# Kernel optimization log

Measured on AMD Instinct MI355X. Metric: run time of the kernel, lower is better.

Reference implementation:

```python
import jax, jax.numpy as jnp
import numpy as np

B = 1024
S_OUT, S_IN, D_IN = 30, 17, 3
H = 4
DKQ_I, DV_I, HID_I, OUT_I = 6, 8, 256, 64
DKQ_O, DV_O, HID_O = 64, 64, 1024
OUT_O = 36 * S_OUT  # 1080


def _mha(x, wq, bq, wk, bk, wv, bv, dkq):
    """Vectorized multi-head self-attention over all heads at once.
    x: [..., P, d_in]; wq/wk: [H, d_in, dkq]; wv: [H, d_in, dv].
    Returns context [..., H, P, dv] (matches torch stack+permute ordering)."""
    q = jnp.einsum('...pd,hdk->...hpk', x, wq) + bq[:, None, :]
    k = jnp.einsum('...pd,hdk->...hpk', x, wk) + bk[:, None, :]
    v = jnp.einsum('...pd,hdv->...hpv', x, wv) + bv[:, None, :]
    scores = jnp.einsum('...hpk,...hqk->...hpq', q, k) / jnp.sqrt(jnp.asarray(dkq, x.dtype))
    attn = jax.nn.softmax(scores, axis=-1)
    return jnp.einsum('...hpq,...hqv->...hpv', attn, v)


def _ml(ctx, w1, b1, w2, b2):
    """MultiHeadLinearLayer: per-head fc1+tanh (shared weights), concat heads, fc2.
    ctx: [..., H, P, dv] -> [..., out]."""
    lead = ctx.shape[:-3]
    flat = ctx.reshape(*lead, H, -1)            # [..., H, P*dv]
    h = jnp.tanh(flat @ w1 + b1)                # [..., H, hidden]
    h = h.reshape(*lead, -1)                    # [..., H*hidden]
    return h @ w2 + b2


def setup_inputs() -> dict:
    key = jax.random.key(0)
    ks = iter(jax.random.split(key, 32))
    n = lambda shape, s=0.05: jax.random.normal(next(ks), shape, dtype=jnp.float32) * s
    inp = {
        'x': jax.random.normal(next(ks), (B, S_OUT, S_IN, D_IN), dtype=jnp.float32),
        # inner multi-head attention (4 heads, stacked weights)
        'iwq': n((H, D_IN, DKQ_I)), 'ibq': n((H, DKQ_I)),
        'iwk': n((H, D_IN, DKQ_I)), 'ibk': n((H, DKQ_I)),
        'iwv': n((H, D_IN, DV_I)),  'ibv': n((H, DV_I)),
        # inner MultiHeadLinearLayer
        'iw1': n((S_IN * DV_I, HID_I)), 'ib1': n((HID_I,)),
        'iw2': n((H * HID_I, OUT_I)),   'ib2': n((OUT_I,)),
        # outer multi-head attention
        'owq': n((H, OUT_I, DKQ_O)), 'obq': n((H, DKQ_O)),
        'owk': n((H, OUT_I, DKQ_O)), 'obk': n((H, DKQ_O)),
        'owv': n((H, OUT_I, DV_O)),  'obv': n((H, DV_O)),
        # outer MultiHeadLinearLayer
        'ow1': n((S_OUT * DV_O, HID_O)), 'ob1': n((HID_O,)),
        'ow2': n((H * HID_O, OUT_O)),    'ob2': n((OUT_O,)),
    }
    return inp


def reference(x, iwq, ibq, iwk, ibk, iwv, ibv, iw1, ib1, iw2, ib2,
              owq, obq, owk, obk, owv, obv, ow1, ob1, ow2, ob2):
    b = x.shape[0]
    # Inner attention applied to all 30 outer positions at once (replaces python loop)
    ctx_i = _mha(x, iwq, ibq, iwk, ibk, iwv, ibv, DKQ_I)      # [B,30,H,17,8]
    seq = _ml(ctx_i, iw1, ib1, iw2, ib2)                       # [B,30,64]
    # Outer attention over the 30-step sequence
    ctx_o = _mha(seq, owq, obq, owk, obk, owv, obv, DKQ_O)     # [B,H,30,64]
    out = _ml(ctx_o, ow1, ob1, ow2, ob2)                       # [B,1080]
    return out.reshape(b, S_OUT, 12, 3)
```

## Files before the change

### kernel.cpp

```cpp
#include <hip/hip_runtime.h>


typedef _Float16 f16x8 __attribute__((ext_vector_type(8)));
typedef _Float16 f16x4 __attribute__((ext_vector_type(4)));
typedef float    f32x4 __attribute__((ext_vector_type(4)));
typedef float    f32x16 __attribute__((ext_vector_type(16)));

union F16x8u { f16x8 v; f16x4 q[2]; };

__device__ inline float tanh_fast(float x) {
    float ax = fabsf(x);
    float e  = __expf(2.0f * ax);
    float r  = 1.0f - 2.0f / (e + 1.0f);
    return copysignf(r, x);
}

__device__ inline f32x16 zero16() {
    f32x16 z;
    #pragma unroll
    for (int i = 0; i < 16; i++) z[i] = 0.f;
    return z;
}

__global__ __launch_bounds__(256) void k_prep_frags(
    const float* __restrict__ iwq, const float* __restrict__ ibq,
    const float* __restrict__ iwk, const float* __restrict__ ibk,
    const float* __restrict__ iwv, const float* __restrict__ ibv,
    _Float16* __restrict__ wqf, _Float16* __restrict__ wkf, _Float16* __restrict__ wvf)
{
    const float SC = 0.40824829046386307f;
    for (int i = threadIdx.x; i < 512; i += 256) {
        const int lanev = i >> 3, jj = i & 7;
        const int n = lanev & 31, grp = lanev >> 5;
        const int h = n >> 3, dk = n & 7;
        float q = 0.f, k = 0.f, v = 0.f;
        if (!grp) {
            if (jj < 3) {
                if (dk < 6) { q = iwq[h*18 + jj*6 + dk] * SC; k = iwk[h*18 + jj*6 + dk]; }
                v = iwv[h*24 + jj*8 + dk];
            } else if (jj == 3) {
                if (dk < 6) { q = ibq[h*6 + dk] * SC; k = ibk[h*6 + dk]; }
                v = ibv[h*8 + dk];
            }
        }
        wqf[i] = (_Float16)q; wkf[i] = (_Float16)k; wvf[i] = (_Float16)v;
    }
}

__global__ __launch_bounds__(256) void k_tcastT(
    const float* __restrict__ W, _Float16* __restrict__ Wt,
    int K, int N, int Kpad)
{
    __shared__ _Float16 tile[64][65];
    const int k0 = blockIdx.x * 64, n0 = blockIdx.y * 64;
    for (int i = threadIdx.x; i < 4096; i += 256) {
        const int r = i >> 6, c = i & 63;
        const int k = k0 + r, n = n0 + c;
        float v = (k < K && n < N) ? W[(size_t)k * N + n] : 0.f;
        tile[c][r] = (_Float16)v;
    }
    __syncthreads();
    for (int i = threadIdx.x; i < 4096; i += 256) {
        const int r = i >> 6, c = i & 63;
        Wt[(size_t)(n0 + r) * Kpad + k0 + c] = tile[r][c];
    }
}

__global__ void k_tcast_iw1(const float* __restrict__ iw1, _Float16* __restrict__ iw1t)
{
    const int n = blockIdx.x;
    const int t = threadIdx.x;
    const int dv = t / 20, p = t % 20;
    float v = (p < 17) ? iw1[(p*8 + dv) * 256 + n] : 0.f;
    iw1t[n * 160 + t] = (_Float16)v;
}

__global__ __launch_bounds__(256) void k_tcast_h(
    const float* __restrict__ W, _Float16* __restrict__ Wt)
{
    const int h = blockIdx.y;
    const int idx = blockIdx.x * 256 + threadIdx.x;
    const int n = idx >> 6, k = idx & 63;
    Wt[h * 4096 + n * 64 + k] = (_Float16)W[h * 4096 + k * 64 + n];
}

__global__ __launch_bounds__(256, 3) void k_inner_attn_mfma(
    const float* __restrict__ x,
    const _Float16* __restrict__ wqf, const _Float16* __restrict__ wkf,
    const _Float16* __restrict__ wvf,
    _Float16* __restrict__ flat)
{
    __shared__ __align__(16) _Float16 lds[4][5248];
    const int t = threadIdx.x, lane = t & 63, w = t >> 6;
    const int l31 = lane & 31, grp = lane >> 5;
    const int bs = blockIdx.x * 4 + w;
    _Float16* kq  = &lds[w][0];
    _Float16* qq  = &lds[w][1152];
    _Float16* vt  = &lds[w][2304];
    _Float16* pf  = &lds[w][3456];
    _Float16* fo2 = &lds[w][4608];

    f16x8 xf;
    #pragma unroll
    for (int i = 0; i < 8; i++) xf[i] = (_Float16)0.f;
    if (grp == 0 && l31 < 17) {
        const float* xr = x + (size_t)bs * 51 + l31 * 3;
        xf[0] = (_Float16)xr[0];
        xf[1] = (_Float16)xr[1];
        xf[2] = (_Float16)xr[2];
        xf[3] = (_Float16)1.0f;
    }
    const f16x8 wq8 = *(const f16x8*)&wqf[lane * 8];
    const f16x8 wk8 = *(const f16x8*)&wkf[lane * 8];
    const f16x8 wv8 = *(const f16x8*)&wvf[lane * 8];

    f32x16 kt = __builtin_amdgcn_mfma_f32_32x32x16_f16(wk8, xf, zero16(), 0, 0, 0);
    f32x16 qt = __builtin_amdgcn_mfma_f32_32x32x16_f16(wq8, xf, zero16(), 0, 0, 0);
    f32x16 vv = __builtin_amdgcn_mfma_f32_32x32x16_f16(xf, wv8, zero16(), 0, 0, 0);

    #pragma unroll
    for (int qd = 0; qd < 4; qd++) {
        const int base = 8 * qd + 4 * grp;
        f16x4 a, b, c;
        #pragma unroll
        for (int i = 0; i < 4; i++) {
            a[i] = (_Float16)kt[4*qd + i];
            b[i] = (_Float16)qt[4*qd + i];
            c[i] = (_Float16)vv[4*qd + i];
        }
        *(f16x4*)&kq[l31 * 36 + base] = a;
        *(f16x4*)&qq[l31 * 36 + base] = b;
        *(f16x4*)&vt[l31 * 36 + base] = c;
    }

    #pragma unroll
    for (int h = 0; h < 4; h++) {
        F16x8u ka, qb;
        #pragma unroll
        for (int i = 0; i < 8; i++) { ka.v[i] = (_Float16)0.f; qb.v[i] = (_Float16)0.f; }
        if (grp == 0) {
            ka.q[0] = *(const f16x4*)&kq[l31 * 36 + h * 8];
            ka.q[1] = *(const f16x4*)&kq[l31 * 36 + h * 8 + 4];
            qb.q[0] = *(const f16x4*)&qq[l31 * 36 + h * 8];
            qb.q[1] = *(const f16x4*)&qq[l31 * 36 + h * 8 + 4];
        }
        f32x16 s = __builtin_amdgcn_mfma_f32_32x32x16_f16(ka.v, qb.v, zero16(), 0, 0, 0);

        float mx = -1e30f;
        #pragma unroll
        for (int r = 0; r < 16; r++) {
            const bool val = (r < 8) || (r == 8 && grp == 0);
            if (val) mx = fmaxf(mx, s[r]);
        }
        mx = fmaxf(mx, __shfl_xor(mx, 32));
        float e[16], sum = 0.f;
        #pragma unroll
        for (int r = 0; r < 16; r++) {
            const bool val = (r < 8) || (r == 8 && grp == 0);
            e[r] = val ? __expf(s[r] - mx) : 0.f;
            sum += e[r];
        }
        sum += __shfl_xor(sum, 32);
        const float inv = __builtin_amdgcn_rcpf(sum);
        #pragma unroll
        for (int qd = 0; qd < 4; qd++) {
            f16x4 pk;
            #pragma unroll
            for (int i = 0; i < 4; i++) pk[i] = (_Float16)(e[4*qd + i] * inv);
            *(f16x4*)&pf[l31 * 36 + 8 * qd + 4 * grp] = pk;
        }

        F16x8u pa1, pa2, vb1, vb2;
        pa1.q[0] = *(const f16x4*)&pf[l31 * 36 + grp * 8];
        pa1.q[1] = *(const f16x4*)&pf[l31 * 36 + grp * 8 + 4];
        pa2.q[0] = *(const f16x4*)&pf[l31 * 36 + 16 + grp * 8];
        pa2.q[1] = *(const f16x4*)&pf[l31 * 36 + 16 + grp * 8 + 4];
        const int vr = (h * 8 + (l31 & 7)) * 36;
        vb1.q[0] = *(const f16x4*)&vt[vr + grp * 8];
        vb1.q[1] = *(const f16x4*)&vt[vr + grp * 8 + 4];
        vb2.q[0] = *(const f16x4*)&vt[vr + 16 + grp * 8];
        vb2.q[1] = *(const f16x4*)&vt[vr + 16 + grp * 8 + 4];
        f32x16 c = __builtin_amdgcn_mfma_f32_32x32x16_f16(pa1.v, vb1.v, zero16(), 0, 0, 0);
        c = __builtin_amdgcn_mfma_f32_32x32x16_f16(pa2.v, vb2.v, c, 0, 0, 0);

        if (l31 < 8) {
            #pragma unroll
            for (int qd = 0; qd < 4; qd++) {
                const int jb = 8 * qd + 4 * grp;
                if (jb < 20) {
                    f16x4 ck;
                    #pragma unroll
                    for (int i = 0; i < 4; i++) ck[i] = (_Float16)c[4*qd + i];
                    *(f16x4*)&fo2[h * 160 + l31 * 20 + jb] = ck;
                }
            }
        }
    }

    _Float16* fg = flat + (size_t)bs * 640;
    *(f16x8*)&fg[lane * 8] = *(const f16x8*)&fo2[lane * 8];
    if (lane < 16)
        *(f16x8*)&fg[512 + lane * 8] = *(const f16x8*)&fo2[512 + lane * 8];
}

__global__ __launch_bounds__(256) void k_inner_ml_mfma(
    const _Float16* __restrict__ flat,
    const _Float16* __restrict__ iw1t,
    const _Float16* __restrict__ iw2t,
    const float* __restrict__ ib1, const float* __restrict__ ib2,
    float* __restrict__ seq)
{
    __shared__ __align__(16) _Float16 h1l[32][1032];
    float* red = (float*)&h1l[0][0];
    const int t = threadIdx.x, lane = t & 63, w = t >> 6;
    const int q = lane >> 4, ml = lane & 15;
    const int m0  = blockIdx.x * 128;
    const int bs0 = blockIdx.x * 32;

    for (int p = 0; p < 2; p++) {
        f32x4 acc[4][4];
        #pragma unroll
        for (int mi = 0; mi < 4; mi++)
            #pragma unroll
            for (int ni = 0; ni < 4; ni++) acc[mi][ni] = (f32x4){0.f,0.f,0.f,0.f};
        for (int ks = 0; ks < 5; ks++) {
            const int k = ks * 32 + q * 8;
            f16x8 a[4], b[4];
            #pragma unroll
            for (int mi = 0; mi < 4; mi++)
                a[mi] = *(const f16x8*)&flat[(size_t)(m0 + p*64 + mi*16 + ml) * 160 + k];
            #pragma unroll
            for (int ni = 0; ni < 4; ni++)
                b[ni] = *(const f16x8*)&iw1t[(size_t)(w*64 + ni*16 + ml) * 160 + k];
            #pragma unroll
            for (int mi = 0; mi < 4; mi++)
                #pragma unroll
                for (int ni = 0; ni < 4; ni++)
                    acc[mi][ni] = __builtin_amdgcn_mfma_f32_16x16x32_f16(a[mi], b[ni], acc[mi][ni], 0, 0, 0);
        }
        #pragma unroll
        for (int mi = 0; mi < 4; mi++)
            #pragma unroll
            for (int ni = 0; ni < 4; ni++)
                #pragma unroll
                for (int r = 0; r < 4; r++) {
                    const int row = p*64 + mi*16 + q*4 + r;
                    const int col = w*64 + ni*16 + ml;
                    const int bs_l = row >> 2, h = row & 3;
                    h1l[bs_l][h*256 + col] = (_Float16)tanh_fast(acc[mi][ni][r] + ib1[col]);
                }
    }
    __syncthreads();

    f32x4 a2[2][4];
    #pragma unroll
    for (int mi = 0; mi < 2; mi++)
        #pragma unroll
        for (int ni = 0; ni < 4; ni++) a2[mi][ni] = (f32x4){0.f,0.f,0.f,0.f};
    for (int ks = 0; ks < 8; ks++) {
        const int k = w * 256 + ks * 32 + q * 8;
        f16x8 a[2], b[4];
        #pragma unroll
        for (int mi = 0; mi < 2; mi++)
            a[mi] = *(const f16x8*)&h1l[mi*16 + ml][k];
        #pragma unroll
        for (int ni = 0; ni < 4; ni++)
            b[ni] = *(const f16x8*)&iw2t[(size_t)(ni*16 + ml) * 1024 + k];
        #pragma unroll
        for (int mi = 0; mi < 2; mi++)
            #pragma unroll
            for (int ni = 0; ni < 4; ni++)
                a2[mi][ni] = __builtin_amdgcn_mfma_f32_16x16x32_f16(a[mi], b[ni], a2[mi][ni], 0, 0, 0);
    }
    __syncthreads();
    #pragma unroll
    for (int mi = 0; mi < 2; mi++)
        #pragma unroll
        for (int ni = 0; ni < 4; ni++)
            #pragma unroll
            for (int r = 0; r < 4; r++) {
                const int row = mi*16 + q*4 + r;
                const int col = ni*16 + ml;
                red[(size_t)w*2048 + row*64 + col] = a2[mi][ni][r];
            }
    __syncthreads();
    for (int i = t; i < 2048; i += 256) {
        const int row = i >> 6, col = i & 63;
        float s = red[i] + red[2048 + i] + red[4096 + i] + red[6144 + i] + ib2[col];
        seq[(size_t)(bs0 + row) * 64 + col] = s;
    }
}

__device__ inline void oa_proj_rows(
    const _Float16 (*seqf)[72], const _Float16* __restrict__ wt,
    const float* __restrict__ bias, _Float16 (*dst)[72], int q, int ml)
{
    f32x4 acc[2][4];
    #pragma unroll
    for (int mi = 0; mi < 2; mi++)
        #pragma unroll
        for (int ni = 0; ni < 4; ni++) acc[mi][ni] = (f32x4){0.f,0.f,0.f,0.f};
    #pragma unroll
    for (int k0 = 0; k0 < 64; k0 += 32) {
        f16x8 a[2], bb[4];
        #pragma unroll
        for (int mi = 0; mi < 2; mi++) a[mi] = *(const f16x8*)&seqf[mi*16 + ml][k0 + q*8];
        #pragma unroll
        for (int ni = 0; ni < 4; ni++) bb[ni] = *(const f16x8*)&wt[(size_t)(ni*16 + ml)*64 + k0 + q*8];
        #pragma unroll
        for (int mi = 0; mi < 2; mi++)
            #pragma unroll
            for (int ni = 0; ni < 4; ni++)
                acc[mi][ni] = __builtin_amdgcn_mfma_f32_16x16x32_f16(a[mi], bb[ni], acc[mi][ni], 0, 0, 0);
    }
    #pragma unroll
    for (int ni = 0; ni < 4; ni++) {
        const float bi = bias[ni*16 + ml];
        #pragma unroll
        for (int mi = 0; mi < 2; mi++)
            #pragma unroll
            for (int r = 0; r < 4; r++)
                dst[mi*16 + q*4 + r][ni*16 + ml] = (_Float16)(acc[mi][ni][r] + bi);
    }
}

__device__ inline void oa_proj_t(
    const _Float16 (*seqf)[72], const _Float16* __restrict__ wt,
    const float* __restrict__ bias, _Float16 (*dstT)[40], int q, int ml)
{
    f32x4 acc[2][4];
    #pragma unroll
    for (int mi = 0; mi < 2; mi++)
        #pragma unroll
        for (int ni = 0; ni < 4; ni++) acc[mi][ni] = (f32x4){0.f,0.f,0.f,0.f};
    #pragma unroll
    for (int k0 = 0; k0 < 64; k0 += 32) {
        f16x8 a[2], bb[4];
        #pragma unroll
        for (int mi = 0; mi < 2; mi++) a[mi] = *(const f16x8*)&seqf[mi*16 + ml][k0 + q*8];
        #pragma unroll
        for (int ni = 0; ni < 4; ni++) bb[ni] = *(const f16x8*)&wt[(size_t)(ni*16 + ml)*64 + k0 + q*8];
        #pragma unroll
        for (int mi = 0; mi < 2; mi++)
            #pragma unroll
            for (int ni = 0; ni < 4; ni++)
                acc[mi][ni] = __builtin_amdgcn_mfma_f32_16x16x32_f16(a[mi], bb[ni], acc[mi][ni], 0, 0, 0);
    }
    #pragma unroll
    for (int ni = 0; ni < 4; ni++) {
        const float bi = bias[ni*16 + ml];
        #pragma unroll
        for (int mi = 0; mi < 2; mi++)
            #pragma unroll
            for (int r = 0; r < 4; r++)
                dstT[ni*16 + ml][mi*16 + q*4 + r] = (_Float16)(acc[mi][ni][r] + bi);
    }
}

__global__ __launch_bounds__(256) void k_outer_attn_mfma(
    const float* __restrict__ seq,
    const _Float16* __restrict__ owqt,
    const _Float16* __restrict__ owkt,
    const _Float16* __restrict__ owvt,
    const float* __restrict__ obq, const float* __restrict__ obk,
    const float* __restrict__ obv,
    _Float16* __restrict__ ctxo)
{
    __shared__ __align__(16) _Float16 seqf[32][72];
    __shared__ __align__(16) _Float16 qf[4][32][72];
    __shared__ __align__(16) _Float16 kf[4][32][72];
    __shared__ __align__(16) _Float16 vt[4][64][40];
    __shared__ __align__(16) _Float16 pf[4][32][40];
    const int t = threadIdx.x, lane = t & 63, w = t >> 6;
    const int q = lane >> 4, ml = lane & 15;
    const int b = blockIdx.x;

    const float* sb = seq + (size_t)b * 1920;
    for (int i = t; i < 2048; i += 256) {
        const int row = i >> 6, col = i & 63;
        seqf[row][col] = (_Float16)(row < 30 ? sb[row*64 + col] : 0.0f);
    }
    __syncthreads();

    oa_proj_rows(seqf, owqt + w*4096, obq + w*64, qf[w], q, ml);
    oa_proj_rows(seqf, owkt + w*4096, obk + w*64, kf[w], q, ml);
    oa_proj_t   (seqf, owvt + w*4096, obv + w*64, vt[w], q, ml);
    __syncthreads();

    f32x4 sc[2][2];
    #pragma unroll
    for (int mi = 0; mi < 2; mi++)
        #pragma unroll
        for (int ni = 0; ni < 2; ni++) sc[mi][ni] = (f32x4){0.f,0.f,0.f,0.f};
    #pragma unroll
    for (int k0 = 0; k0 < 64; k0 += 32) {
        f16x8 aq[2], bk[2];
        #pragma unroll
        for (int mi = 0; mi < 2; mi++) aq[mi] = *(const f16x8*)&qf[w][mi*16 + ml][k0 + q*8];
        #pragma unroll
        for (int ni = 0; ni < 2; ni++) bk[ni] = *(const f16x8*)&kf[w][ni*16 + ml][k0 + q*8];
        #pragma unroll
        for (int mi = 0; mi < 2; mi++)
            #pragma unroll
            for (int ni = 0; ni < 2; ni++)
                sc[mi][ni] = __builtin_amdgcn_mfma_f32_16x16x32_f16(aq[mi], bk[ni], sc[mi][ni], 0, 0, 0);
    }

    const bool maskhi = (ml >= 14);
    #pragma unroll
    for (int mi = 0; mi < 2; mi++) {
        #pragma unroll
        for (int r = 0; r < 4; r++) {
            const float s0 = sc[mi][0][r] * 0.125f;
            const float s1 = maskhi ? -1e30f : sc[mi][1][r] * 0.125f;
            float mx = fmaxf(s0, s1);
            #pragma unroll
            for (int off = 1; off < 16; off <<= 1) mx = fmaxf(mx, __shfl_xor(mx, off, 64));
            const float e0 = __expf(s0 - mx);
            const float e1 = __expf(s1 - mx);
            float sm = e0 + e1;
            #pragma unroll
            for (int off = 1; off < 16; off <<= 1) sm += __shfl_xor(sm, off, 64);
            const float inv = 1.0f / sm;
            pf[w][mi*16 + q*4 + r][ml]      = (_Float16)(e0 * inv);
            pf[w][mi*16 + q*4 + r][16 + ml] = (_Float16)(e1 * inv);
        }
    }
    __syncthreads();

    f16x8 ap[2], bv[4];
    #pragma unroll
    for (int mi = 0; mi < 2; mi++) ap[mi] = *(const f16x8*)&pf[w][mi*16 + ml][q*8];
    #pragma unroll
    for (int ni = 0; ni < 4; ni++) bv[ni] = *(const f16x8*)&vt[w][ni*16 + ml][q*8];
    f32x4 oa[2][4];
    #pragma unroll
    for (int mi = 0; mi < 2; mi++)
        #pragma unroll
        for (int ni = 0; ni < 4; ni++) {
            oa[mi][ni] = (f32x4){0.f,0.f,0.f,0.f};
            oa[mi][ni] = __builtin_amdgcn_mfma_f32_16x16x32_f16(ap[mi], bv[ni], oa[mi][ni], 0, 0, 0);
        }

    _Float16* co = ctxo + (size_t)(b*4 + w) * 1920;
    #pragma unroll
    for (int mi = 0; mi < 2; mi++)
        #pragma unroll
        for (int r = 0; r < 4; r++) {
            const int row = mi*16 + q*4 + r;
            if (row < 30) {
                #pragma unroll
                for (int ni = 0; ni < 4; ni++)
                    co[row*64 + ni*16 + ml] = (_Float16)oa[mi][ni][r];
            }
        }
}

__global__ __launch_bounds__(128) void k_outer_fc1_mfma(
    const _Float16* __restrict__ ctxo,
    const _Float16* __restrict__ ow1t,
    const float* __restrict__ ob1,
    _Float16* __restrict__ hout)
{
    __shared__ float red[2][64][65];
    const int t = threadIdx.x, lane = t & 63, w = t >> 6;
    const int q = lane >> 4, ml = lane & 15;
    const int M0 = (blockIdx.x >> 4) * 64;
    const int N0 = (blockIdx.x & 15) * 64;
    f32x4 acc[4][4];
    #pragma unroll
    for (int mi = 0; mi < 4; mi++)
        #pragma unroll
        for (int ni = 0; ni < 4; ni++) acc[mi][ni] = (f32x4){0.f,0.f,0.f,0.f};
    for (int ks = 0; ks < 30; ks++) {
        const int k = w * 960 + ks * 32 + q * 8;
        f16x8 a[4], b[4];
        #pragma unroll
        for (int mi = 0; mi < 4; mi++)
            a[mi] = *(const f16x8*)&ctxo[(size_t)(M0 + mi*16 + ml) * 1920 + k];
        #pragma unroll
        for (int ni = 0; ni < 4; ni++)
            b[ni] = *(const f16x8*)&ow1t[(size_t)(N0 + ni*16 + ml) * 1920 + k];
        #pragma unroll
        for (int mi = 0; mi < 4; mi++)
            #pragma unroll
            for (int ni = 0; ni < 4; ni++)
                acc[mi][ni] = __builtin_amdgcn_mfma_f32_16x16x32_f16(a[mi], b[ni], acc[mi][ni], 0, 0, 0);
    }
    #pragma unroll
    for (int mi = 0; mi < 4; mi++)
        #pragma unroll
        for (int ni = 0; ni < 4; ni++)
            #pragma unroll
            for (int r = 0; r < 4; r++)
                red[w][mi*16 + q*4 + r][ni*16 + ml] = acc[mi][ni][r];
    __syncthreads();
    for (int i = t; i < 4096; i += 128) {
        const int row = i >> 6, col = i & 63;
        const float s = red[0][row][col] + red[1][row][col] + ob1[N0 + col];
        hout[(size_t)(M0 + row) * 1024 + N0 + col] = (_Float16)tanh_fast(s);
    }
}

__global__ __launch_bounds__(256) void k_outer_fc2_mfma(
    const _Float16* __restrict__ hout,
    const _Float16* __restrict__ ow2t,
    const float* __restrict__ ob2,
    float* __restrict__ out)
{
    __shared__ float red[4][32][65];
    const int t = threadIdx.x, lane = t & 63, w = t >> 6;
    const int q = lane >> 4, ml = lane & 15;
    const int M0 = (blockIdx.x / 17) * 32;
    const int N0 = (blockIdx.x % 17) * 64;
    f32x4 acc[2][4];
    #pragma unroll
    for (int mi = 0; mi < 2; mi++)
        #pragma unroll
        for (int ni = 0; ni < 4; ni++) acc[mi][ni] = (f32x4){0.f,0.f,0.f,0.f};
    for (int ks = 0; ks < 32; ks++) {
        const int k = w * 1024 + ks * 32 + q * 8;
        f16x8 a[2], b[4];
        #pragma unroll
        for (int mi = 0; mi < 2; mi++)
            a[mi] = *(const f16x8*)&hout[(size_t)(M0 + mi*16 + ml) * 4096 + k];
        #pragma unroll
        for (int ni = 0; ni < 4; ni++)
            b[ni] = *(const f16x8*)&ow2t[(size_t)(N0 + ni*16 + ml) * 4096 + k];
        #pragma unroll
        for (int mi = 0; mi < 2; mi++)
            #pragma unroll
            for (int ni = 0; ni < 4; ni++)
                acc[mi][ni] = __builtin_amdgcn_mfma_f32_16x16x32_f16(a[mi], b[ni], acc[mi][ni], 0, 0, 0);
    }
    #pragma unroll
    for (int mi = 0; mi < 2; mi++)
        #pragma unroll
        for (int ni = 0; ni < 4; ni++)
            #pragma unroll
            for (int r = 0; r < 4; r++)
                red[w][mi*16 + q*4 + r][ni*16 + ml] = acc[mi][ni][r];
    __syncthreads();
    for (int i = t; i < 2048; i += 256) {
        const int row = i >> 6, col = i & 63;
        const int n = N0 + col;
        if (n < 1080) {
            float s = red[0][row][col] + red[1][row][col] + red[2][row][col] + red[3][row][col] + ob2[n];
            out[(size_t)(M0 + row) * 1080 + n] = s;
        }
    }
}

extern "C" void kernel_launch(void* const* d_in, const int* in_sizes, int n_in,
                              void* d_out, int out_size, void* d_ws, size_t ws_size,
                              hipStream_t stream) {
    const float* x   = (const float*)d_in[0];
    const float* iwq = (const float*)d_in[1];
    const float* ibq = (const float*)d_in[2];
    const float* iwk = (const float*)d_in[3];
    const float* ibk = (const float*)d_in[4];
    const float* iwv = (const float*)d_in[5];
    const float* ibv = (const float*)d_in[6];
    const float* iw1 = (const float*)d_in[7];
    const float* ib1 = (const float*)d_in[8];
    const float* iw2 = (const float*)d_in[9];
    const float* ib2 = (const float*)d_in[10];
    const float* owq = (const float*)d_in[11];
    const float* obq = (const float*)d_in[12];
    const float* owk = (const float*)d_in[13];
    const float* obk = (const float*)d_in[14];
    const float* owv = (const float*)d_in[15];
    const float* obv = (const float*)d_in[16];
    const float* ow1 = (const float*)d_in[17];
    const float* ob1 = (const float*)d_in[18];
    const float* ow2 = (const float*)d_in[19];
    const float* ob2 = (const float*)d_in[20];

    char* ws = (char*)d_ws;
    _Float16* iw1t   = (_Float16*)(ws + 0);
    _Float16* wqf    = (_Float16*)(ws + 98304);
    _Float16* wkf    = (_Float16*)(ws + 99328);
    _Float16* wvf    = (_Float16*)(ws + 100352);
    _Float16* iw2t   = (_Float16*)(ws + 163840);
    _Float16* ow1t   = (_Float16*)(ws + 294912);
    _Float16* ow2t   = (_Float16*)(ws + 4227072);
    _Float16* flat   = (_Float16*)(ws + 13139968);
    float*    seq    = (float*)   (ws + 52461568);
    _Float16* owqt   = (_Float16*)(ws + 60325888);
    _Float16* owkt   = (_Float16*)(ws + 60358656);
    _Float16* owvt   = (_Float16*)(ws + 60391424);
    _Float16* ctxo   = (_Float16*)(ws + 13139968);
    _Float16* houtb  = (_Float16*)(ws + 28868608);
    float*    out    = (float*)d_out;

    k_prep_frags<<<dim3(1), dim3(256), 0, stream>>>(iwq, ibq, iwk, ibk, iwv, ibv, wqf, wkf, wvf);
    k_tcast_iw1 <<<dim3(256), dim3(160), 0, stream>>>(iw1, iw1t);
    k_tcastT<<<dim3(16, 1),  dim3(256), 0, stream>>>(iw2, iw2t, 1024, 64, 1024);
    k_tcastT<<<dim3(30, 16), dim3(256), 0, stream>>>(ow1, ow1t, 1920, 1024, 1920);
    k_tcastT<<<dim3(64, 17), dim3(256), 0, stream>>>(ow2, ow2t, 4096, 1080, 4096);
    k_tcast_h<<<dim3(16, 4), dim3(256), 0, stream>>>(owq, owqt);
    k_tcast_h<<<dim3(16, 4), dim3(256), 0, stream>>>(owk, owkt);
    k_tcast_h<<<dim3(16, 4), dim3(256), 0, stream>>>(owv, owvt);

    k_inner_attn_mfma<<<dim3(7680), dim3(256), 0, stream>>>(x, wqf, wkf, wvf, flat);
    k_inner_ml_mfma  <<<dim3(960),  dim3(256), 0, stream>>>(flat, iw1t, iw2t, ib1, ib2, seq);
    k_outer_attn_mfma<<<dim3(1024), dim3(256), 0, stream>>>(seq, owqt, owkt, owvt, obq, obk, obv, ctxo);
    k_outer_fc1_mfma <<<dim3(1024), dim3(128), 0, stream>>>(ctxo, ow1t, ob1, houtb);
    k_outer_fc2_mfma <<<dim3(544),  dim3(256), 0, stream>>>(houtb, ow2t, ob2, out);
}
```

Baseline: 374.7 us.

## Fuse weight prep kernels, double-buffer GEMM loads, split-K outer fc2

Merges the eight weight-cast/transpose launches into a single block-dispatched kernel. The outer fc1 and fc2 GEMMs now prefetch the next K-step's fragments into registers while issuing MFMAs on the current step. The fc2 GEMM is split four ways along K to launch four times as many blocks. Fp32 partials go to workspace and a separate reduction kernel adds them with the bias. This targets launch overhead and low occupancy/latency exposure in fc2, at the cost of extra partial-sum memory traffic, another launch, and more registers for double-buffering.

```diff
diff --git a/kernel.cpp b/kernel.cpp
--- a/kernel.cpp
+++ b/kernel.cpp
@@ -22,66 +22,85 @@
     return z;
 }
 
-__global__ __launch_bounds__(256) void k_prep_frags(
-    const float* __restrict__ iwq, const float* __restrict__ ibq,
-    const float* __restrict__ iwk, const float* __restrict__ ibk,
-    const float* __restrict__ iwv, const float* __restrict__ ibv,
-    _Float16* __restrict__ wqf, _Float16* __restrict__ wkf, _Float16* __restrict__ wvf)
-{
-    const float SC = 0.40824829046386307f;
-    for (int i = threadIdx.x; i < 512; i += 256) {
-        const int lanev = i >> 3, jj = i & 7;
-        const int n = lanev & 31, grp = lanev >> 5;
-        const int h = n >> 3, dk = n & 7;
-        float q = 0.f, k = 0.f, v = 0.f;
-        if (!grp) {
-            if (jj < 3) {
-                if (dk < 6) { q = iwq[h*18 + jj*6 + dk] * SC; k = iwk[h*18 + jj*6 + dk]; }
-                v = iwv[h*24 + jj*8 + dk];
-            } else if (jj == 3) {
-                if (dk < 6) { q = ibq[h*6 + dk] * SC; k = ibk[h*6 + dk]; }
-                v = ibv[h*8 + dk];
-            }
-        }
-        wqf[i] = (_Float16)q; wkf[i] = (_Float16)k; wvf[i] = (_Float16)v;
-    }
-}
-
-__global__ __launch_bounds__(256) void k_tcastT(
+__device__ inline void tcast_tile(
     const float* __restrict__ W, _Float16* __restrict__ Wt,
-    int K, int N, int Kpad)
-{
-    __shared__ _Float16 tile[64][65];
-    const int k0 = blockIdx.x * 64, n0 = blockIdx.y * 64;
-    for (int i = threadIdx.x; i < 4096; i += 256) {
+    int tileIdx, int nkx, int K, int N, int Kpad,
+    _Float16 (*tile)[65], int t)
+{
+    const int kx = tileIdx % nkx, ny = tileIdx / nkx;
+    const int k0 = kx * 64, n0 = ny * 64;
+    for (int i = t; i < 4096; i += 256) {
         const int r = i >> 6, c = i & 63;
         const int k = k0 + r, n = n0 + c;
         float v = (k < K && n < N) ? W[(size_t)k * N + n] : 0.f;
         tile[c][r] = (_Float16)v;
     }
     __syncthreads();
-    for (int i = threadIdx.x; i < 4096; i += 256) {
+    for (int i = t; i < 4096; i += 256) {
         const int r = i >> 6, c = i & 63;
         Wt[(size_t)(n0 + r) * Kpad + k0 + c] = tile[r][c];
     }
 }
 
-__global__ void k_tcast_iw1(const float* __restrict__ iw1, _Float16* __restrict__ iw1t)
-{
-    const int n = blockIdx.x;
-    const int t = threadIdx.x;
-    const int dv = t / 20, p = t % 20;
-    float v = (p < 17) ? iw1[(p*8 + dv) * 256 + n] : 0.f;
-    iw1t[n * 160 + t] = (_Float16)v;
-}
-
-__global__ __launch_bounds__(256) void k_tcast_h(
-    const float* __restrict__ W, _Float16* __restrict__ Wt)
-{
-    const int h = blockIdx.y;
-    const int idx = blockIdx.x * 256 + threadIdx.x;
-    const int n = idx >> 6, k = idx & 63;
-    Wt[h * 4096 + n * 64 + k] = (_Float16)W[h * 4096 + k * 64 + n];
+__global__ __launch_bounds__(256) void k_prep_all(
+    const float* __restrict__ iwq, const float* __restrict__ ibq,
+    const float* __restrict__ iwk, const float* __restrict__ ibk,
+    const float* __restrict__ iwv, const float* __restrict__ ibv,
+    const float* __restrict__ iw1, const float* __restrict__ iw2,
+    const float* __restrict__ ow1, const float* __restrict__ ow2,
+    const float* __restrict__ owq, const float* __restrict__ owk,
+    const float* __restrict__ owv,
+    _Float16* __restrict__ wqf, _Float16* __restrict__ wkf,
+    _Float16* __restrict__ wvf,
+    _Float16* __restrict__ iw1t, _Float16* __restrict__ iw2t,
+    _Float16* __restrict__ ow1t, _Float16* __restrict__ ow2t,
+    _Float16* __restrict__ owqt, _Float16* __restrict__ owkt,
+    _Float16* __restrict__ owvt)
+{
+    __shared__ _Float16 tile[64][65];
+    const int b = blockIdx.x, t = threadIdx.x;
+    if (b == 0) {
+        const float SC = 0.40824829046386307f;
+        for (int i = t; i < 512; i += 256) {
+            const int lanev = i >> 3, jj = i & 7;
+            const int n = lanev & 31, grp = lanev >> 5;
+            const int h = n >> 3, dk = n & 7;
+            float q = 0.f, k = 0.f, v = 0.f;
+            if (!grp) {
+                if (jj < 3) {
+                    if (dk < 6) { q = iwq[h*18 + jj*6 + dk] * SC; k = iwk[h*18 + jj*6 + dk]; }
+                    v = iwv[h*24 + jj*8 + dk];
+                } else if (jj == 3) {
+                    if (dk < 6) { q = ibq[h*6 + dk] * SC; k = ibk[h*6 + dk]; }
+                    v = ibv[h*8 + dk];
+                }
+            }
+            wqf[i] = (_Float16)q; wkf[i] = (_Float16)k; wvf[i] = (_Float16)v;
+        }
+    } else if (b < 161) {
+        const int idx = (b - 1) * 256 + t;
+        if (idx < 40960) {
+            const int n = idx / 160, kp = idx - n * 160;
+            const int dv = kp / 20, p = kp - dv * 20;
+            float v = (p < 17) ? iw1[(p*8 + dv) * 256 + n] : 0.f;
+            iw1t[n * 160 + kp] = (_Float16)v;
+        }
+    } else if (b < 177) {
+        tcast_tile(iw2, iw2t, b - 161, 16, 1024, 64, 1024, tile, t);
+    } else if (b < 657) {
+        tcast_tile(ow1, ow1t, b - 177, 30, 1920, 1024, 1920, tile, t);
+    } else if (b < 1745) {
+        tcast_tile(ow2, ow2t, b - 657, 64, 4096, 1080, 4096, tile, t);
+    } else {
+        const int s = b - 1745;
+        const int mat = s >> 6, rem = s & 63;
+        const int h = rem >> 4, blk = rem & 15;
+        const int idx = blk * 256 + t;
+        const int n = idx >> 6, k = idx & 63;
+        const float* W = (mat == 0) ? owq : (mat == 1) ? owk : owv;
+        _Float16* Wt   = (mat == 0) ? owqt : (mat == 1) ? owkt : owvt;
+        Wt[h * 4096 + n * 64 + k] = (_Float16)W[h * 4096 + k * 64 + n];
+    }
 }
 
 __global__ __launch_bounds__(256, 3) void k_inner_attn_mfma(
@@ -467,25 +486,36 @@
     const int q = lane >> 4, ml = lane & 15;
     const int M0 = (blockIdx.x >> 4) * 64;
     const int N0 = (blockIdx.x & 15) * 64;
+    const int kk0 = w * 960 + q * 8;
     f32x4 acc[4][4];
     #pragma unroll
     for (int mi = 0; mi < 4; mi++)
         #pragma unroll
         for (int ni = 0; ni < 4; ni++) acc[mi][ni] = (f32x4){0.f,0.f,0.f,0.f};
+    f16x8 a[2][4], b[2][4];
+    #pragma unroll
+    for (int mi = 0; mi < 4; mi++)
+        a[0][mi] = *(const f16x8*)&ctxo[(size_t)(M0 + mi*16 + ml) * 1920 + kk0];
+    #pragma unroll
+    for (int ni = 0; ni < 4; ni++)
+        b[0][ni] = *(const f16x8*)&ow1t[(size_t)(N0 + ni*16 + ml) * 1920 + kk0];
+    #pragma unroll
     for (int ks = 0; ks < 30; ks++) {
-        const int k = w * 960 + ks * 32 + q * 8;
-        f16x8 a[4], b[4];
+        const int cur = ks & 1, nxt = cur ^ 1;
+        if (ks < 29) {
+            const int kn = kk0 + (ks + 1) * 32;
+            #pragma unroll
+            for (int mi = 0; mi < 4; mi++)
+                a[nxt][mi] = *(const f16x8*)&ctxo[(size_t)(M0 + mi*16 + ml) * 1920 + kn];
+            #pragma unroll
+            for (int ni = 0; ni < 4; ni++)
+                b[nxt][ni] = *(const f16x8*)&ow1t[(size_t)(N0 + ni*16 + ml) * 1920 + kn];
+        }
         #pragma unroll
         for (int mi = 0; mi < 4; mi++)
-            a[mi] = *(const f16x8*)&ctxo[(size_t)(M0 + mi*16 + ml) * 1920 + k];
-        #pragma unroll
-        for (int ni = 0; ni < 4; ni++)
-            b[ni] = *(const f16x8*)&ow1t[(size_t)(N0 + ni*16 + ml) * 1920 + k];
-        #pragma unroll
-        for (int mi = 0; mi < 4; mi++)
-            #pragma unroll
-            for (int ni = 0; ni < 4; ni++)
-                acc[mi][ni] = __builtin_amdgcn_mfma_f32_16x16x32_f16(a[mi], b[ni], acc[mi][ni], 0, 0, 0);
+            #pragma unroll
+            for (int ni = 0; ni < 4; ni++)
+                acc[mi][ni] = __builtin_amdgcn_mfma_f32_16x16x32_f16(a[cur][mi], b[cur][ni], acc[mi][ni], 0, 0, 0);
     }
     #pragma unroll
     for (int mi = 0; mi < 4; mi++)
@@ -505,33 +535,46 @@
 __global__ __launch_bounds__(256) void k_outer_fc2_mfma(
     const _Float16* __restrict__ hout,
     const _Float16* __restrict__ ow2t,
-    const float* __restrict__ ob2,
-    float* __restrict__ out)
+    float* __restrict__ part)
 {
     __shared__ float red[4][32][65];
     const int t = threadIdx.x, lane = t & 63, w = t >> 6;
     const int q = lane >> 4, ml = lane & 15;
-    const int M0 = (blockIdx.x / 17) * 32;
-    const int N0 = (blockIdx.x % 17) * 64;
+    const int bid = blockIdx.x;
+    const int kc = bid & 3;
+    const int rest = bid >> 2;
+    const int M0 = (rest / 17) * 32;
+    const int N0 = (rest % 17) * 64;
+    const int kk0 = kc * 1024 + w * 256 + q * 8;
     f32x4 acc[2][4];
     #pragma unroll
     for (int mi = 0; mi < 2; mi++)
         #pragma unroll
         for (int ni = 0; ni < 4; ni++) acc[mi][ni] = (f32x4){0.f,0.f,0.f,0.f};
-    for (int ks = 0; ks < 32; ks++) {
-        const int k = w * 1024 + ks * 32 + q * 8;
-        f16x8 a[2], b[4];
-        #pragma unroll
-        for (int mi = 0; mi < 2; mi++)
-            a[mi] = *(const f16x8*)&hout[(size_t)(M0 + mi*16 + ml) * 4096 + k];
-        #pragma unroll
-        for (int ni = 0; ni < 4; ni++)
-            b[ni] = *(const f16x8*)&ow2t[(size_t)(N0 + ni*16 + ml) * 4096 + k];
-        #pragma unroll
-        for (int mi = 0; mi < 2; mi++)
-            #pragma unroll
-            for (int ni = 0; ni < 4; ni++)
-                acc[mi][ni] = __builtin_amdgcn_mfma_f32_16x16x32_f16(a[mi], b[ni], acc[mi][ni], 0, 0, 0);
+    f16x8 a[2][2], b[2][4];
+    #pragma unroll
+    for (int mi = 0; mi < 2; mi++)
+        a[0][mi] = *(const f16x8*)&hout[(size_t)(M0 + mi*16 + ml) * 4096 + kk0];
+    #pragma unroll
+    for (int ni = 0; ni < 4; ni++)
+        b[0][ni] = *(const f16x8*)&ow2t[(size_t)(N0 + ni*16 + ml) * 4096 + kk0];
+    #pragma unroll
+    for (int ks = 0; ks < 8; ks++) {
+        const int cur = ks & 1, nxt = cur ^ 1;
+        if (ks < 7) {
+            const int kn = kk0 + (ks + 1) * 32;
+            #pragma unroll
+            for (int mi = 0; mi < 2; mi++)
+                a[nxt][mi] = *(const f16x8*)&hout[(size_t)(M0 + mi*16 + ml) * 4096 + kn];
+            #pragma unroll
+            for (int ni = 0; ni < 4; ni++)
+                b[nxt][ni] = *(const f16x8*)&ow2t[(size_t)(N0 + ni*16 + ml) * 4096 + kn];
+        }
+        #pragma unroll
+        for (int mi = 0; mi < 2; mi++)
+            #pragma unroll
+            for (int ni = 0; ni < 4; ni++)
+                acc[mi][ni] = __builtin_amdgcn_mfma_f32_16x16x32_f16(a[cur][mi], b[cur][ni], acc[mi][ni], 0, 0, 0);
     }
     #pragma unroll
     for (int mi = 0; mi < 2; mi++)
@@ -545,10 +588,21 @@
         const int row = i >> 6, col = i & 63;
         const int n = N0 + col;
         if (n < 1080) {
-            float s = red[0][row][col] + red[1][row][col] + red[2][row][col] + red[3][row][col] + ob2[n];
-            out[(size_t)(M0 + row) * 1080 + n] = s;
-        }
-    }
+            const float s = red[0][row][col] + red[1][row][col] + red[2][row][col] + red[3][row][col];
+            part[(size_t)kc * 1105920 + (size_t)(M0 + row) * 1080 + n] = s;
+        }
+    }
+}
+
+__global__ __launch_bounds__(256) void k_fc2_reduce(
+    const float* __restrict__ part, const float* __restrict__ ob2,
+    float* __restrict__ out)
+{
+    const int idx = blockIdx.x * 256 + threadIdx.x;
+    if (idx >= 1105920) return;
+    const int n = idx % 1080;
+    out[idx] = part[idx] + part[1105920 + idx] + part[2211840 + idx]
+             + part[3317760 + idx] + ob2[n];
 }
 
 extern "C" void kernel_launch(void* const* d_in, const int* in_sizes, int n_in,
@@ -590,21 +644,17 @@
     _Float16* owkt   = (_Float16*)(ws + 60358656);
     _Float16* owvt   = (_Float16*)(ws + 60391424);
     _Float16* ctxo   = (_Float16*)(ws + 13139968);
-    _Float16* houtb  = (_Float16*)(ws + 28868608);
+    float*    part   = (float*)   (ws + 13139968);
+    _Float16* houtb  = (_Float16*)(ws + 40000000);
     float*    out    = (float*)d_out;
 
-    k_prep_frags<<<dim3(1), dim3(256), 0, stream>>>(iwq, ibq, iwk, ibk, iwv, ibv, wqf, wkf, wvf);
-    k_tcast_iw1 <<<dim3(256), dim3(160), 0, stream>>>(iw1, iw1t);
-    k_tcastT<<<dim3(16, 1),  dim3(256), 0, stream>>>(iw2, iw2t, 1024, 64, 1024);
-    k_tcastT<<<dim3(30, 16), dim3(256), 0, stream>>>(ow1, ow1t, 1920, 1024, 1920);
-    k_tcastT<<<dim3(64, 17), dim3(256), 0, stream>>>(ow2, ow2t, 4096, 1080, 4096);
-    k_tcast_h<<<dim3(16, 4), dim3(256), 0, stream>>>(owq, owqt);
-    k_tcast_h<<<dim3(16, 4), dim3(256), 0, stream>>>(owk, owkt);
-    k_tcast_h<<<dim3(16, 4), dim3(256), 0, stream>>>(owv, owvt);
-
+    k_prep_all       <<<dim3(1937), dim3(256), 0, stream>>>(
+        iwq, ibq, iwk, ibk, iwv, ibv, iw1, iw2, ow1, ow2, owq, owk, owv,
+        wqf, wkf, wvf, iw1t, iw2t, ow1t, ow2t, owqt, owkt, owvt);
     k_inner_attn_mfma<<<dim3(7680), dim3(256), 0, stream>>>(x, wqf, wkf, wvf, flat);
     k_inner_ml_mfma  <<<dim3(960),  dim3(256), 0, stream>>>(flat, iw1t, iw2t, ib1, ib2, seq);
     k_outer_attn_mfma<<<dim3(1024), dim3(256), 0, stream>>>(seq, owqt, owkt, owvt, obq, obk, obv, ctxo);
     k_outer_fc1_mfma <<<dim3(1024), dim3(128), 0, stream>>>(ctxo, ow1t, ob1, houtb);
-    k_outer_fc2_mfma <<<dim3(544),  dim3(256), 0, stream>>>(houtb, ow2t, ob2, out);
-}
+    k_outer_fc2_mfma <<<dim3(2176), dim3(256), 0, stream>>>(houtb, ow2t, part);
+    k_fc2_reduce     <<<dim3(4320), dim3(256), 0, stream>>>(part, ob2, out);
+}
```

Measured after the change: 335.2 us. 1.12x faster.
